# Performance work log

Hardware: AMD Instinct MI355X
Metric: run time of the kernel (lower is better)

Reference implementation:

```python
import jax, jax.numpy as jnp
import numpy as np

N, E, B, DIM = 10000, 100000, 64, 64
NF, EF, H = 92, 50, 128
N_CONV, STEPS = 2, 2


def setup_inputs() -> dict:
    key = jax.random.key(0)
    ks = jax.random.split(key, 16)
    r = lambda k, s: jax.random.normal(k, s, dtype=jnp.float32) * 0.05
    return {
        "x": jax.random.normal(ks[0], (N, NF), dtype=jnp.float32),
        "edge_attr": jax.random.normal(ks[1], (E, EF), dtype=jnp.float32),
        "lin0_w": r(ks[2], (DIM, NF)), "lin0_b": jnp.zeros((DIM,), jnp.float32),
        "nn1_w": r(ks[3], (H, EF)), "nn1_b": jnp.zeros((H,), jnp.float32),
        "nn2_w": r(ks[4], (DIM * DIM, H)), "nn2_b": jnp.zeros((DIM * DIM,), jnp.float32),
        "root": r(ks[5], (DIM, DIM)), "conv_bias": jnp.zeros((DIM,), jnp.float32),
        "gru_w_ih": r(ks[6], (3 * DIM, DIM)), "gru_w_hh": r(ks[7], (3 * DIM, DIM)),
        "gru_b_ih": jnp.zeros((3 * DIM,), jnp.float32), "gru_b_hh": jnp.zeros((3 * DIM,), jnp.float32),
        "lstm_w_ih": r(ks[8], (4 * DIM, 2 * DIM)), "lstm_w_hh": r(ks[9], (4 * DIM, DIM)),
        "lstm_b_ih": jnp.zeros((4 * DIM,), jnp.float32), "lstm_b_hh": jnp.zeros((4 * DIM,), jnp.float32),
        "lin1_w": r(ks[10], (DIM, 2 * DIM)), "lin1_b": jnp.zeros((DIM,), jnp.float32),
        "lin2_w": r(ks[11], (1, DIM)), "lin2_b": jnp.zeros((1,), jnp.float32),
        "edge_index": jax.random.randint(ks[12], (2, E), 0, N),
        "batch": jnp.sort(jax.random.randint(ks[13], (N,), 0, B)),
    }


def _forward(x, edge_attr, lin0_w, lin0_b, nn1_w, nn1_b, nn2_w, nn2_b, root, conv_bias,
             gru_w_ih, gru_w_hh, gru_b_ih, gru_b_hh, lstm_w_ih, lstm_w_hh, lstm_b_ih, lstm_b_hh,
             lin1_w, lin1_b, lin2_w, lin2_b, edge_index, batch):
    src, dst = edge_index[0], edge_index[1]
    out = jax.nn.relu(x @ lin0_w.T + lin0_b)            # [N, DIM]
    h = out                                              # GRU hidden state (h0 = out)
    # Edge-conditioned weights depend only on edge_attr; identical each conv step.
    he = jax.nn.relu(edge_attr @ nn1_w.T + nn1_b)        # [E, H]
    We = (he @ nn2_w.T + nn2_b).reshape(E, DIM, DIM)     # [E, DIM, DIM]
    deg = jax.ops.segment_sum(jnp.ones((E,), jnp.float32), dst, num_segments=N)
    inv_deg = jnp.where(deg > 0, 1.0 / jnp.maximum(deg, 1.0), 0.0)[:, None]
    for _ in range(N_CONV):
        msg = jnp.einsum('ei,eio->eo', out[src], We)     # per-edge matvec, [E, DIM]
        agg = jax.ops.segment_sum(msg, dst, num_segments=N) * inv_deg  # scatter-mean
        m = jax.nn.relu(agg + out @ root + conv_bias)
        # GRU cell (torch gate order: r, z, n)
        gx = m @ gru_w_ih.T + gru_b_ih
        gh = h @ gru_w_hh.T + gru_b_hh
        xr, xz, xn = jnp.split(gx, 3, axis=-1)
        hr, hz, hn = jnp.split(gh, 3, axis=-1)
        rg = jax.nn.sigmoid(xr + hr)
        zg = jax.nn.sigmoid(xz + hz)
        ng = jnp.tanh(xn + rg * hn)
        h = (1.0 - zg) * ng + zg * h
        out = h
    # Set2Set pooling
    q_star = jnp.zeros((B, 2 * DIM), jnp.float32)
    hs = jnp.zeros((B, DIM), jnp.float32)
    cs = jnp.zeros((B, DIM), jnp.float32)
    for _ in range(STEPS):
        gates = q_star @ lstm_w_ih.T + lstm_b_ih + hs @ lstm_w_hh.T + lstm_b_hh
        ig, fg, gg, og = jnp.split(gates, 4, axis=-1)    # torch gate order i,f,g,o
        cs = jax.nn.sigmoid(fg) * cs + jax.nn.sigmoid(ig) * jnp.tanh(gg)
        hs = jax.nn.sigmoid(og) * jnp.tanh(cs)
        q = hs                                           # [B, DIM]
        e = jnp.sum(out * q[batch], axis=-1)             # [N]
        emax = jax.ops.segment_max(e, batch, num_segments=B)
        ee = jnp.exp(e - emax[batch])
        denom = jax.ops.segment_sum(ee, batch, num_segments=B)
        a = ee / jnp.maximum(denom, 1e-16)[batch]        # per-graph softmax
        rvec = jax.ops.segment_sum(a[:, None] * out, batch, num_segments=B)
        q_star = jnp.concatenate([q, rvec], axis=-1)     # [B, 2*DIM]
    y = jax.nn.relu(q_star @ lin1_w.T + lin1_b) @ lin2_w.T + lin2_b
    return y.reshape(-1)                                 # [B]


def reference(x, edge_attr, lin0_w, lin0_b, nn1_w, nn1_b, nn2_w, nn2_b, root, conv_bias,
              gru_w_ih, gru_w_hh, gru_b_ih, gru_b_hh, lstm_w_ih, lstm_w_hh, lstm_b_ih, lstm_b_hh,
              lin1_w, lin1_b, lin2_w, lin2_b, edge_index, batch):
    return _forward(x, edge_attr, lin0_w, lin0_b, nn1_w, nn1_b, nn2_w, nn2_b, root, conv_bias,
                    gru_w_ih, gru_w_hh, gru_b_ih, gru_b_hh, lstm_w_ih, lstm_w_hh, lstm_b_ih, lstm_b_hh,
                    lin1_w, lin1_b, lin2_w, lin2_b, edge_index, batch)
```

## Files before the change

### kernel.cpp

```cpp
#include <hip/hip_runtime.h>
#include <hip/hip_bf16.h>

#define N_   10000
#define E_   100000
#define B_   64
#define DIM_ 64
#define NF_  92
#define EF_  50
#define H_   128

typedef unsigned int u32;

__device__ __forceinline__ float sigm(float x) { return 1.f / (1.f + __expf(-x)); }
__device__ __forceinline__ float rdlane(float v, int l) {
  return __uint_as_float(__builtin_amdgcn_readlane(__float_as_uint(v), l));
}

__global__ __launch_bounds__(256) void k_lin0(const float* __restrict__ x,
                                              const float* __restrict__ w,
                                              const float* __restrict__ b,
                                              float* __restrict__ out) {
  __shared__ float xs[4][NF_];
  __shared__ float w_s[DIM_][93];
  int n0 = blockIdx.x << 2;
  int tid = threadIdx.x;
  for (int k = tid; k < 4 * NF_; k += 256) {
    int nl = k / NF_, f = k % NF_;
    xs[nl][f] = x[(size_t)(n0 + nl) * NF_ + f];
  }
  for (int g = tid; g < DIM_ * NF_; g += 256) {
    int d = g / NF_, f = g % NF_;
    w_s[d][f] = w[g];
  }
  __syncthreads();
  int nl = tid >> 6, d = tid & 63;
  float acc = b[d];
  for (int f = 0; f < NF_; ++f) acc += xs[nl][f] * w_s[d][f];
  out[(size_t)(n0 + nl) * DIM_ + d] = fmaxf(acc, 0.f);
}

__global__ __launch_bounds__(256) void k_he(const float* __restrict__ ea,
                                            const float* __restrict__ w,
                                            const float* __restrict__ b,
                                            float* __restrict__ he) {
  __shared__ float wt[EF_][132];
  __shared__ float es[32][52];
  int e0 = blockIdx.x * 32, t = threadIdx.x;
  for (int g = t; g < H_ * EF_; g += 256) {
    int h = g / EF_, f = g % EF_;
    wt[f][h] = w[g];
  }
  for (int g = t; g < 32 * EF_; g += 256) {
    int e = g / EF_, f = g % EF_;
    es[e][f] = ea[(size_t)(e0 + e) * EF_ + f];
  }
  __syncthreads();
  int h0 = (t & 31) << 2, eg = t >> 5;
  float acc[4][4];
#pragma unroll
  for (int j = 0; j < 4; ++j)
#pragma unroll
    for (int c = 0; c < 4; ++c) acc[j][c] = b[h0 + c];
  for (int f = 0; f < EF_; ++f) {
    float4 wv = *(const float4*)&wt[f][h0];
    const float* wp = (const float*)&wv;
#pragma unroll
    for (int j = 0; j < 4; ++j) {
      float ev = es[eg * 4 + j][f];
#pragma unroll
      for (int c = 0; c < 4; ++c) acc[j][c] = fmaf(ev, wp[c], acc[j][c]);
    }
  }
#pragma unroll
  for (int j = 0; j < 4; ++j) {
    float4 o;
    o.x = fmaxf(acc[j][0], 0.f); o.y = fmaxf(acc[j][1], 0.f);
    o.z = fmaxf(acc[j][2], 0.f); o.w = fmaxf(acc[j][3], 0.f);
    *(float4*)&he[(size_t)(e0 + eg * 4 + j) * H_ + h0] = o;
  }
}

__global__ __launch_bounds__(256) void k_hist(const int* __restrict__ ei,
                                              int* __restrict__ outcnt,
                                              float* __restrict__ degf) {
  int e = blockIdx.x * 256 + threadIdx.x;
  if (e < E_) {
    atomicAdd(&outcnt[ei[e]], 1);
    atomicAdd(&degf[ei[E_ + e]], 1.0f);
  }
}

__global__ __launch_bounds__(1024) void k_scan(const int* __restrict__ outcnt,
                                               int* __restrict__ estart,
                                               int* __restrict__ cursor) {
  __shared__ int part[1024];
  int t = threadIdx.x;
  int base = t * 10;
  int c[10];
  int s = 0;
#pragma unroll
  for (int j = 0; j < 10; ++j) {
    int idx = base + j;
    c[j] = (idx < N_) ? outcnt[idx] : 0;
    s += c[j];
  }
  part[t] = s;
  __syncthreads();
  for (int off = 1; off < 1024; off <<= 1) {
    int v = (t >= off) ? part[t - off] : 0;
    __syncthreads();
    part[t] += v;
    __syncthreads();
  }
  int ex = (t > 0) ? part[t - 1] : 0;
#pragma unroll
  for (int j = 0; j < 10; ++j) {
    int idx = base + j;
    if (idx < N_) { estart[idx] = ex; cursor[idx] = ex; }
    ex += c[j];
  }
  if (t == 1023) estart[N_] = part[1023];
}

__global__ __launch_bounds__(256) void k_scatter(const int* __restrict__ ei,
                                                 int* __restrict__ cursor,
                                                 int* __restrict__ eorder) {
  int e = blockIdx.x * 256 + threadIdx.x;
  if (e < E_) {
    int s = ei[e];
    int pos = atomicAdd(&cursor[s], 1);
    eorder[pos] = e;
  }
}

__global__ __launch_bounds__(256) void k_gstart(const int* __restrict__ batch,
                                                int* __restrict__ gs) {
  int n = blockIdx.x * 256 + threadIdx.x;
  if (n >= N_) return;
  int b = batch[n];
  if (n == 0) {
    for (int bb = 0; bb <= b; ++bb) gs[bb] = 0;
  } else {
    int pb = batch[n - 1];
    if (pb != b)
      for (int bb = pb + 1; bb <= b; ++bb) gs[bb] = n;
  }
  if (n == N_ - 1) {
    for (int bb = b + 1; bb <= B_; ++bb) gs[bb] = N_;
  }
}

__global__ __launch_bounds__(256) void k_transpose(const float* __restrict__ gih,
                                                   const float* __restrict__ ghh,
                                                   const float* __restrict__ lih,
                                                   const float* __restrict__ lhh,
                                                   float* __restrict__ gihT,
                                                   float* __restrict__ ghhT,
                                                   float* __restrict__ lihT,
                                                   float* __restrict__ lhhT) {
  int idx = blockIdx.x * 256 + threadIdx.x;
  if (idx < 192 * 64) {
    int r = idx >> 6, i = idx & 63;
    gihT[i * 192 + r] = gih[idx];
    ghhT[i * 192 + r] = ghh[idx];
  }
  if (idx < 256 * 128) {
    int r = idx >> 7, k = idx & 127;
    lihT[k * 256 + r] = lih[idx];
  }
  if (idx < 256 * 64) {
    int r = idx >> 6, k = idx & 63;
    lhhT[k * 256 + r] = lhh[idx];
  }
}

__global__ __launch_bounds__(256) void k_vgemm(const float* __restrict__ outv,
                                               const float* __restrict__ nn2w,
                                               float* __restrict__ V4,
                                               int h_base, int H4Cbuf, int lwHg) {
  __shared__ float a_s[128][64];
  __shared__ float b_s[64][128];
  int n0 = blockIdx.x << 7;
  int og = blockIdx.y >> lwHg;
  int hg = blockIdx.y & ((1 << lwHg) - 1);
  int o0 = og << 4;
  int h0 = h_base + (hg << 3);
  int t = threadIdx.x;
#pragma unroll
  for (int k = 0; k < 8; ++k) {
    int idx = t + (k << 8);
    int nl = idx >> 4, i0 = (idx & 15) << 2;
    float4 v = make_float4(0.f, 0.f, 0.f, 0.f);
    int n = n0 + nl;
    if (n < N_) v = *(const float4*)&outv[(size_t)n * 64 + i0];
    int sh = 2 * nl;
    int c0 = (i0 + sh) & 63;
    a_s[nl][c0] = v.x; a_s[nl][c0 + 1] = v.y;
    int c2 = (i0 + 2 + sh) & 63;
    a_s[nl][c2] = v.z; a_s[nl][c2 + 1] = v.w;
  }
#pragma unroll
  for (int k = 0; k < 8; ++k) {
    int idx = t + (k << 8);
    int i = idx >> 5, c0 = (idx & 31) << 2;
    int o = o0 + (c0 >> 3);
    int hh = h0 + (c0 & 7);
    *(float4*)&b_s[i][c0] = *(const float4*)&nn2w[((size_t)((i << 6) + o)) * 128 + hh];
  }
  __syncthreads();
  int tx = t & 15, ty = t >> 4;
  float acc[8][8];
#pragma unroll
  for (int r = 0; r < 8; ++r)
#pragma unroll
    for (int c = 0; c < 8; ++c) acc[r][c] = 0.f;
#pragma unroll 4
  for (int i = 0; i < 64; i += 2) {
    float2 a2[8];
#pragma unroll
    for (int r = 0; r < 8; ++r) {
      int row = ty * 8 + r;
      a2[r] = *(const float2*)&a_s[row][(i + 2 * row) & 63];
    }
    float4 b00 = *(const float4*)&b_s[i][tx << 2];
    float4 b01 = *(const float4*)&b_s[i][64 + (tx << 2)];
    float4 b10 = *(const float4*)&b_s[i + 1][tx << 2];
    float4 b11 = *(const float4*)&b_s[i + 1][64 + (tx << 2)];
    const float* p00 = (const float*)&b00;
    const float* p01 = (const float*)&b01;
    const float* p10 = (const float*)&b10;
    const float* p11 = (const float*)&b11;
#pragma unroll
    for (int r = 0; r < 8; ++r) {
      float ax = a2[r].x, ay = a2[r].y;
#pragma unroll
      for (int c = 0; c < 4; ++c) {
        acc[r][c]     = fmaf(ax, p00[c], acc[r][c]);
        acc[r][c]     = fmaf(ay, p10[c], acc[r][c]);
        acc[r][4 + c] = fmaf(ax, p01[c], acc[r][4 + c]);
        acc[r][4 + c] = fmaf(ay, p11[c], acc[r][4 + c]);
      }
    }
  }
  float4* V4v = (float4*)V4;
  int h4 = (hg << 1) + (tx & 1);
  int olo = o0 + (tx >> 1);
#pragma unroll
  for (int r = 0; r < 8; ++r) {
    int n = n0 + ty * 8 + r;
    if (n >= N_) continue;
    float4 lo = make_float4(acc[r][0], acc[r][1], acc[r][2], acc[r][3]);
    float4 hi = make_float4(acc[r][4], acc[r][5], acc[r][6], acc[r][7]);
    size_t base = ((size_t)n * H4Cbuf + h4) * 64;
    V4v[base + olo]     = lo;
    V4v[base + olo + 8] = hi;
  }
}

__global__ __launch_bounds__(256) void k_bt(const float* __restrict__ out,
                                            const float* __restrict__ nn2b,
                                            float* __restrict__ bt) {
  __shared__ float os[4][64];
  int n0 = blockIdx.x << 2;
  int tid = threadIdx.x;
  int nl = tid >> 6, o = tid & 63;
  os[nl][o] = out[(size_t)(n0 + nl) * 64 + o];
  __syncthreads();
  float acc = 0.f;
  for (int i = 0; i < 64; ++i) acc += os[nl][i] * nn2b[(i << 6) + o];
  bt[(size_t)(n0 + nl) * 64 + o] = acc;
}

template <int H4C>
__global__ __launch_bounds__(256) void k_edge(const float* __restrict__ V4,
                                              const float* __restrict__ he,
                                              const float* __restrict__ bt,
                                              const int* __restrict__ ei,
                                              const int* __restrict__ estart,
                                              const int* __restrict__ eorder,
                                              float* __restrict__ agg,
                                              int hofs) {
  int wid = threadIdx.x >> 6, lane = threadIdx.x & 63;
  int n = blockIdx.x * 4 + wid;
  if (n >= N_) return;
  int se = estart[n], ee = estart[n + 1];
  if (se == ee) return;
  const float4* vp = (const float4*)V4 + (size_t)n * H4C * 64 + lane;
  float4 v4[H4C];
#pragma unroll
  for (int h4 = 0; h4 < H4C; ++h4) v4[h4] = vp[(size_t)h4 * 64];
  float btv = (hofs == 0) ? bt[(size_t)n * 64 + lane] : 0.f;
  constexpr int CWm1 = 4 * H4C - 1;
  for (int q = se; q < ee; ++q) {
    int eid = eorder[q];
    int dst = ei[E_ + eid];
    const float* hep = &he[(size_t)eid * H_];
    float hh, hh2 = 0.f;
    if (H4C == 32) { hh = hep[lane]; hh2 = hep[64 + lane]; }
    else           { hh = hep[hofs + (lane & CWm1)]; }
    float acc = btv;
#pragma unroll
    for (int h4 = 0; h4 < H4C; ++h4) {
      const float* vv = (const float*)&v4[h4];
#pragma unroll
      for (int c = 0; c < 4; ++c) {
        int hl = h4 * 4 + c;
        float bh = (hl < 64) ? rdlane(hh, hl) : rdlane(hh2, hl - 64);
        acc = fmaf(bh, vv[c], acc);
      }
    }
    atomicAdd(&agg[(size_t)dst * 64 + lane], acc);
  }
}

__global__ __launch_bounds__(256) void k_update(const float* __restrict__ agg,
                                                const float* __restrict__ deg,
                                                const float* __restrict__ cur,
                                                const float* __restrict__ root,
                                                const float* __restrict__ cbias,
                                                const float* __restrict__ wihT,
                                                const float* __restrict__ whhT,
                                                const float* __restrict__ bih,
                                                const float* __restrict__ bhh,
                                                float* __restrict__ nxt) {
  __shared__ float outs[32][64];
  __shared__ float ms[32][64];
  int n0 = blockIdx.x << 5;
  int tid = threadIdx.x;
  int o = tid & 63, g = tid >> 6;
#pragma unroll
  for (int k = 0; k < 8; ++k) {
    int idx = tid + (k << 8);
    int nl = idx >> 6, i = idx & 63;
    int n = n0 + nl;
    outs[nl][i] = (n < N_) ? cur[(size_t)n * 64 + i] : 0.f;
  }
  __syncthreads();
  float acc[8];
  float cb = cbias[o];
#pragma unroll
  for (int j = 0; j < 8; ++j) {
    int n = n0 + (g << 3) + j;
    if (n < N_) {
      float dg = deg[n];
      float iv = dg > 0.f ? 1.f / dg : 0.f;
      acc[j] = agg[(size_t)n * 64 + o] * iv + cb;
    } else acc[j] = 0.f;
  }
  for (int i = 0; i < 64; ++i) {
    float r = root[(i << 6) + o];
#pragma unroll
    for (int j = 0; j < 8; ++j) acc[j] = fmaf(outs[(g << 3) + j][i], r, acc[j]);
  }
#pragma unroll
  for (int j = 0; j < 8; ++j) ms[(g << 3) + j][o] = fmaxf(acc[j], 0.f);
  __syncthreads();
  float xr[8], xz[8], xn[8], hr[8], hz[8], hn[8];
  {
    float br = bih[o], bz = bih[64 + o], bn = bih[128 + o];
    float dr = bhh[o], dz = bhh[64 + o], dn = bhh[128 + o];
#pragma unroll
    for (int j = 0; j < 8; ++j) {
      xr[j] = br; xz[j] = bz; xn[j] = bn;
      hr[j] = dr; hz[j] = dz; hn[j] = dn;
    }
  }
  for (int i = 0; i < 64; ++i) {
    const float* wi = &wihT[i * 192];
    const float* vi = &whhT[i * 192];
    float w0 = wi[o], w1 = wi[64 + o], w2 = wi[128 + o];
    float v0 = vi[o], v1 = vi[64 + o], v2 = vi[128 + o];
#pragma unroll
    for (int j = 0; j < 8; ++j) {
      int nl = (g << 3) + j;
      float mi = ms[nl][i], hi = outs[nl][i];
      xr[j] = fmaf(mi, w0, xr[j]);
      xz[j] = fmaf(mi, w1, xz[j]);
      xn[j] = fmaf(mi, w2, xn[j]);
      hr[j] = fmaf(hi, v0, hr[j]);
      hz[j] = fmaf(hi, v1, hz[j]);
      hn[j] = fmaf(hi, v2, hn[j]);
    }
  }
#pragma unroll
  for (int j = 0; j < 8; ++j) {
    int nl = (g << 3) + j;
    int n = n0 + nl;
    if (n < N_) {
      float rg = sigm(xr[j] + hr[j]);
      float zg = sigm(xz[j] + hz[j]);
      float ng = tanhf(xn[j] + rg * hn[j]);
      nxt[(size_t)n * 64 + o] = (1.f - zg) * ng + zg * outs[nl][o];
    }
  }
}

__global__ __launch_bounds__(256) void k_s2s(const float* __restrict__ out,
                                             const int* __restrict__ gs,
                                             float* __restrict__ qstar,
                                             float* __restrict__ hs,
                                             float* __restrict__ cs,
                                             const float* __restrict__ lihT,
                                             const float* __restrict__ lhhT,
                                             const float* __restrict__ bih,
                                             const float* __restrict__ bhh,
                                             const float* __restrict__ w1,
                                             const float* __restrict__ b1,
                                             const float* __restrict__ w2,
                                             const float* __restrict__ b2,
                                             float* __restrict__ y, int dofinal) {
  int b = blockIdx.x, tid = threadIdx.x;
  __shared__ float qs[128];
  __shared__ float hss[64];
  __shared__ float gsh[256];
  __shared__ float qv[64];
  __shared__ float rv[64];
  __shared__ float wred[4];
  __shared__ float rred[4][64];
  if (tid < 128) qs[tid] = qstar[b * 128 + tid];
  else if (tid < 192) hss[tid - 128] = hs[b * 64 + (tid - 128)];
  __syncthreads();
  {
    int r = tid;
    float acc = bih[r] + bhh[r];
    for (int k = 0; k < 128; ++k) acc += qs[k] * lihT[k * 256 + r];
    for (int k = 0; k < 64; ++k) acc += hss[k] * lhhT[k * 256 + r];
    gsh[r] = acc;
  }
  __syncthreads();
  if (tid < 64) {
    float ig = sigm(gsh[tid]), fg = sigm(gsh[64 + tid]);
    float gg = tanhf(gsh[128 + tid]), og = sigm(gsh[192 + tid]);
    float c = fg * cs[b * 64 + tid] + ig * gg;
    cs[b * 64 + tid] = c;
    float hv = og * tanhf(c);
    hs[b * 64 + tid] = hv;
    qv[tid] = hv;
  }
  __syncthreads();
  int wid = tid >> 6, l = tid & 63;
  int s = gs[b], e_ = gs[b + 1];
  float wmax = -3.4e38f;
  for (int n = s + wid; n < e_; n += 4) {
    float p = out[(size_t)n * 64 + l] * qv[l];
#pragma unroll
    for (int off = 32; off; off >>= 1) p += __shfl_xor(p, off);
    wmax = fmaxf(wmax, p);
  }
  if (l == 0) wred[wid] = wmax;
  __syncthreads();
  float gmax = fmaxf(fmaxf(wred[0], wred[1]), fmaxf(wred[2], wred[3]));
  __syncthreads();
  float dacc = 0.f, racc = 0.f;
  for (int n = s + wid; n < e_; n += 4) {
    float p = out[(size_t)n * 64 + l] * qv[l];
#pragma unroll
    for (int off = 32; off; off >>= 1) p += __shfl_xor(p, off);
    float ee = __expf(p - gmax);
    dacc += ee;
    racc += ee * out[(size_t)n * 64 + l];
  }
  rred[wid][l] = racc;
  if (l == 0) wred[wid] = dacc;
  __syncthreads();
  if (wid == 0) {
    float denom = wred[0] + wred[1] + wred[2] + wred[3];
    float r = (rred[0][l] + rred[1][l] + rred[2][l] + rred[3][l]) /
              fmaxf(denom, 1e-16f);
    rv[l] = r;
    qstar[b * 128 + l] = qv[l];
    qstar[b * 128 + 64 + l] = r;
  }
  if (dofinal) {
    __syncthreads();
    if (tid < 64) {
      float acc = b1[tid];
      for (int k = 0; k < 64; ++k) acc += qv[k] * w1[tid * 128 + k];
      for (int k = 0; k < 64; ++k) acc += rv[k] * w1[tid * 128 + 64 + k];
      float t1 = fmaxf(acc, 0.f) * w2[tid];
#pragma unroll
      for (int off = 32; off; off >>= 1) t1 += __shfl_xor(t1, off);
      if (tid == 0) y[b] = t1 + b2[0];
    }
  }
}

extern "C" void kernel_launch(void* const* d_in, const int* in_sizes, int n_in,
                              void* d_out, int out_size, void* d_ws, size_t ws_size,
                              hipStream_t stream) {
  const float* x        = (const float*)d_in[0];
  const float* ea       = (const float*)d_in[1];
  const float* lin0_w   = (const float*)d_in[2];
  const float* lin0_b   = (const float*)d_in[3];
  const float* nn1_w    = (const float*)d_in[4];
  const float* nn1_b    = (const float*)d_in[5];
  const float* nn2_w    = (const float*)d_in[6];
  const float* nn2_b    = (const float*)d_in[7];
  const float* root     = (const float*)d_in[8];
  const float* cbias    = (const float*)d_in[9];
  const float* gru_wih  = (const float*)d_in[10];
  const float* gru_whh  = (const float*)d_in[11];
  const float* gru_bih  = (const float*)d_in[12];
  const float* gru_bhh  = (const float*)d_in[13];
  const float* lstm_wih = (const float*)d_in[14];
  const float* lstm_whh = (const float*)d_in[15];
  const float* lstm_bih = (const float*)d_in[16];
  const float* lstm_bhh = (const float*)d_in[17];
  const float* lin1_w   = (const float*)d_in[18];
  const float* lin1_b   = (const float*)d_in[19];
  const float* lin2_w   = (const float*)d_in[20];
  const float* lin2_b   = (const float*)d_in[21];
  const int*   ei       = (const int*)d_in[22];
  const int*   batch    = (const int*)d_in[23];
  float* yout = (float*)d_out;
  (void)n_in; (void)in_sizes; (void)out_size;

  size_t off = 0;
  auto carve = [&](size_t bytes) -> void* {
    void* p = (char*)d_ws + off;
    off = (off + bytes + 255) & ~(size_t)255;
    return p;
  };
  float* deg    = (float*)carve((size_t)N_ * 4);
  int*   outcnt = (int*)carve((size_t)N_ * 4);
  float* qstar  = (float*)carve((size_t)B_ * 128 * 4);
  float* hs     = (float*)carve((size_t)B_ * 64 * 4);
  float* cs     = (float*)carve((size_t)B_ * 64 * 4);
  size_t zero_span = off;
  float* out_a  = (float*)carve((size_t)N_ * DIM_ * 4);
  float* out_b  = (float*)carve((size_t)N_ * DIM_ * 4);
  float* bt     = (float*)carve((size_t)N_ * DIM_ * 4);
  float* agg    = (float*)carve((size_t)N_ * DIM_ * 4);
  int*   estart = (int*)carve((size_t)(N_ + 1) * 4);
  int*   cursor = (int*)carve((size_t)N_ * 4);
  int*   eorder = (int*)carve((size_t)E_ * 4);
  int*   gs     = (int*)carve((size_t)(B_ + 1) * 4);
  float* gihT   = (float*)carve((size_t)192 * 64 * 4);
  float* ghhT   = (float*)carve((size_t)192 * 64 * 4);
  float* lihT   = (float*)carve((size_t)256 * 128 * 4);
  float* lhhT   = (float*)carve((size_t)256 * 64 * 4);
  float* he     = (float*)carve((size_t)E_ * H_ * 4);
  size_t common = off;
  int CW = 8;
  {
    const int cws[4] = {64, 32, 16, 8};
    for (int i = 0; i < 4; ++i) {
      size_t vb = (size_t)N_ * cws[i] * 64 * 4;
      if (common + vb <= ws_size) { CW = cws[i]; break; }
    }
  }
  float* V4 = (float*)carve((size_t)N_ * CW * 64 * 4);
  int nchunks = 128 / CW;
  int lwHg = __builtin_ctz(CW >> 3);
  int H4Cb = CW / 4;

  hipMemsetAsync(d_ws, 0, zero_span, stream);

  k_lin0<<<N_ / 4, 256, 0, stream>>>(x, lin0_w, lin0_b, out_a);
  k_he<<<E_ / 32, 256, 0, stream>>>(ea, nn1_w, nn1_b, he);
  k_hist<<<(E_ + 255) / 256, 256, 0, stream>>>(ei, outcnt, deg);
  k_scan<<<1, 1024, 0, stream>>>(outcnt, estart, cursor);
  k_scatter<<<(E_ + 255) / 256, 256, 0, stream>>>(ei, cursor, eorder);
  k_gstart<<<(N_ + 255) / 256, 256, 0, stream>>>(batch, gs);
  k_transpose<<<128, 256, 0, stream>>>(gru_wih, gru_whh, lstm_wih, lstm_whh,
                                       gihT, ghhT, lihT, lhhT);

  float* cur = out_a;
  float* nxt = out_b;
  int ntile = (N_ + 127) / 128;
  dim3 vg(ntile, 4 << lwHg);
  int egrid = (N_ + 3) / 4;
  for (int t = 0; t < 2; ++t) {
    hipMemsetAsync(agg, 0, (size_t)N_ * DIM_ * 4, stream);
    k_bt<<<N_ / 4, 256, 0, stream>>>(cur, nn2_b, bt);
    for (int chunk = 0; chunk < nchunks; ++chunk) {
      int h_base = chunk * CW;
      k_vgemm<<<vg, 256, 0, stream>>>(cur, nn2_w, V4, h_base, H4Cb, lwHg);
      switch (CW) {
        case 64:  k_edge<16><<<egrid, 256, 0, stream>>>(V4, he, bt, ei, estart, eorder, agg, h_base); break;
        case 32:  k_edge<8><<<egrid, 256, 0, stream>>>(V4, he, bt, ei, estart, eorder, agg, h_base); break;
        case 16:  k_edge<4><<<egrid, 256, 0, stream>>>(V4, he, bt, ei, estart, eorder, agg, h_base); break;
        default:  k_edge<2><<<egrid, 256, 0, stream>>>(V4, he, bt, ei, estart, eorder, agg, h_base); break;
      }
    }
    k_update<<<(N_ + 31) / 32, 256, 0, stream>>>(agg, deg, cur, root, cbias,
                                                 gihT, ghhT, gru_bih, gru_bhh, nxt);
    float* tmp = cur; cur = nxt; nxt = tmp;
  }

  k_s2s<<<B_, 256, 0, stream>>>(cur, gs, qstar, hs, cs, lihT, lhhT,
                                lstm_bih, lstm_bhh, lin1_w, lin1_b, lin2_w,
                                lin2_b, yout, 0);
  k_s2s<<<B_, 256, 0, stream>>>(cur, gs, qstar, hs, cs, lihT, lhhT,
                                lstm_bih, lstm_bhh, lin1_w, lin1_b, lin2_w,
                                lin2_b, yout, 1);
}
```

Before: 908.6 us.

## Replace FP32 node-weight GEMM with split-bf16 MFMA GEMM

Replaces the scalar FP32 shared-memory GEMM that builds per-node V tensors with a matrix-core kernel using bf16 MFMA instructions. Both operands are split into high and low bf16 parts (three MFMAs per tile) to approximate FP32 accuracy, and nn2_w is pre-transposed and pre-split once into a chunked layout. The activations are split each conv step by a new kernel. This trades extra conversion passes, extra workspace and a small loss of precision for much higher matrix throughput.

Measured after the change: 817.8 us. 1.11x faster.

```diff
diff --git a/kernel.cpp b/kernel.cpp
--- a/kernel.cpp
+++ b/kernel.cpp
@@ -8,12 +8,24 @@
 #define NF_  92
 #define EF_  50
 #define H_   128
+#define NPAD 10048
 
 typedef unsigned int u32;
+typedef unsigned short u16;
+typedef __attribute__((ext_vector_type(8))) short s16x8;
+typedef __attribute__((ext_vector_type(4))) float f32x4;
 
 __device__ __forceinline__ float sigm(float x) { return 1.f / (1.f + __expf(-x)); }
 __device__ __forceinline__ float rdlane(float v, int l) {
   return __uint_as_float(__builtin_amdgcn_readlane(__float_as_uint(v), l));
+}
+__device__ __forceinline__ float bf2f(u16 u) {
+  return __uint_as_float(((u32)u) << 16);
+}
+__device__ __forceinline__ u16 f2bf(float f) {
+  u32 u = __float_as_uint(f);
+  u32 r = (u + 0x7FFFu + ((u >> 16) & 1u)) >> 16;
+  return (u16)r;
 }
 
 __global__ __launch_bounds__(256) void k_lin0(const float* __restrict__ x,
@@ -174,87 +186,96 @@
   }
 }
 
-__global__ __launch_bounds__(256) void k_vgemm(const float* __restrict__ outv,
-                                               const float* __restrict__ nn2w,
-                                               float* __restrict__ V4,
-                                               int h_base, int H4Cbuf, int lwHg) {
-  __shared__ float a_s[128][64];
-  __shared__ float b_s[64][128];
-  int n0 = blockIdx.x << 7;
-  int og = blockIdx.y >> lwHg;
-  int hg = blockIdx.y & ((1 << lwHg) - 1);
-  int o0 = og << 4;
-  int h0 = h_base + (hg << 3);
-  int t = threadIdx.x;
-#pragma unroll
-  for (int k = 0; k < 8; ++k) {
-    int idx = t + (k << 8);
-    int nl = idx >> 4, i0 = (idx & 15) << 2;
-    float4 v = make_float4(0.f, 0.f, 0.f, 0.f);
-    int n = n0 + nl;
-    if (n < N_) v = *(const float4*)&outv[(size_t)n * 64 + i0];
-    int sh = 2 * nl;
-    int c0 = (i0 + sh) & 63;
-    a_s[nl][c0] = v.x; a_s[nl][c0 + 1] = v.y;
-    int c2 = (i0 + 2 + sh) & 63;
-    a_s[nl][c2] = v.z; a_s[nl][c2 + 1] = v.w;
-  }
-#pragma unroll
-  for (int k = 0; k < 8; ++k) {
-    int idx = t + (k << 8);
-    int i = idx >> 5, c0 = (idx & 31) << 2;
-    int o = o0 + (c0 >> 3);
-    int hh = h0 + (c0 & 7);
-    *(float4*)&b_s[i][c0] = *(const float4*)&nn2w[((size_t)((i << 6) + o)) * 128 + hh];
-  }
-  __syncthreads();
-  int tx = t & 15, ty = t >> 4;
-  float acc[8][8];
-#pragma unroll
-  for (int r = 0; r < 8; ++r)
-#pragma unroll
-    for (int c = 0; c < 8; ++c) acc[r][c] = 0.f;
-#pragma unroll 4
-  for (int i = 0; i < 64; i += 2) {
-    float2 a2[8];
-#pragma unroll
-    for (int r = 0; r < 8; ++r) {
-      int row = ty * 8 + r;
-      a2[r] = *(const float2*)&a_s[row][(i + 2 * row) & 63];
-    }
-    float4 b00 = *(const float4*)&b_s[i][tx << 2];
-    float4 b01 = *(const float4*)&b_s[i][64 + (tx << 2)];
-    float4 b10 = *(const float4*)&b_s[i + 1][tx << 2];
-    float4 b11 = *(const float4*)&b_s[i + 1][64 + (tx << 2)];
-    const float* p00 = (const float*)&b00;
-    const float* p01 = (const float*)&b01;
-    const float* p10 = (const float*)&b10;
-    const float* p11 = (const float*)&b11;
-#pragma unroll
-    for (int r = 0; r < 8; ++r) {
-      float ax = a2[r].x, ay = a2[r].y;
-#pragma unroll
-      for (int c = 0; c < 4; ++c) {
-        acc[r][c]     = fmaf(ax, p00[c], acc[r][c]);
-        acc[r][c]     = fmaf(ay, p10[c], acc[r][c]);
-        acc[r][4 + c] = fmaf(ax, p01[c], acc[r][4 + c]);
-        acc[r][4 + c] = fmaf(ay, p11[c], acc[r][4 + c]);
+__global__ __launch_bounds__(256) void k_prep_w(const float* __restrict__ w,
+                                                u16* __restrict__ bth,
+                                                u16* __restrict__ btl,
+                                                int CW) {
+  int idx = blockIdx.x * 256 + threadIdx.x;
+  if (idx >= 64 * 64 * 128) return;
+  int h = idx & 127;
+  int io = idx >> 7;
+  int o = io & 63;
+  int i = io >> 6;
+  int chunk = h / CW, hl = h % CW;
+  float v = w[idx];
+  u16 hh = f2bf(v);
+  float r = v - bf2f(hh);
+  size_t dst = (size_t)chunk * CW * 4096 + ((size_t)(hl * 64 + o)) * 64 + i;
+  bth[dst] = hh;
+  btl[dst] = f2bf(r);
+}
+
+__global__ __launch_bounds__(256) void k_split_a(const float* __restrict__ src,
+                                                 u16* __restrict__ hi,
+                                                 u16* __restrict__ lo) {
+  int idx = blockIdx.x * 256 + threadIdx.x;
+  if (idx >= NPAD * 64) return;
+  float v = (idx < N_ * 64) ? src[idx] : 0.f;
+  u16 h = f2bf(v);
+  float r = v - bf2f(h);
+  hi[idx] = h;
+  lo[idx] = f2bf(r);
+}
+
+__global__ __launch_bounds__(256) void k_vgemm_mfma(const u16* __restrict__ Ah,
+                                                    const u16* __restrict__ Al,
+                                                    const u16* __restrict__ BTh,
+                                                    const u16* __restrict__ BTl,
+                                                    float* __restrict__ V4,
+                                                    int H4Cb) {
+  int n0 = blockIdx.x << 6;
+  int by = blockIdx.y;
+  int tid = threadIdx.x;
+  int w = tid >> 6, l = tid & 63;
+  int lr = l & 15, lg = l >> 4;
+  int o0 = w << 4;
+  int h0 = by << 2;
+  f32x4 acc[4][4];
+#pragma unroll
+  for (int nt = 0; nt < 4; ++nt)
+#pragma unroll
+    for (int t = 0; t < 4; ++t) acc[nt][t] = (f32x4){0.f, 0.f, 0.f, 0.f};
+#pragma unroll
+  for (int ks = 0; ks < 2; ++ks) {
+    int kk = (lg << 3) + (ks << 5);
+    s16x8 ah[4], al[4];
+#pragma unroll
+    for (int nt = 0; nt < 4; ++nt) {
+      size_t ao = (size_t)(n0 + (nt << 4) + lr) * 64 + kk;
+      ah[nt] = *(const s16x8*)(Ah + ao);
+      al[nt] = *(const s16x8*)(Al + ao);
+    }
+    s16x8 bh[4], bl[4];
+#pragma unroll
+    for (int t = 0; t < 4; ++t) {
+      size_t bo = (size_t)(((h0 + t) << 6) + o0 + lr) * 64 + kk;
+      bh[t] = *(const s16x8*)(BTh + bo);
+      bl[t] = *(const s16x8*)(BTl + bo);
+    }
+#pragma unroll
+    for (int nt = 0; nt < 4; ++nt)
+#pragma unroll
+      for (int t = 0; t < 4; ++t) {
+        acc[nt][t] = __builtin_amdgcn_mfma_f32_16x16x32_bf16(ah[nt], bh[t], acc[nt][t], 0, 0, 0);
+        acc[nt][t] = __builtin_amdgcn_mfma_f32_16x16x32_bf16(ah[nt], bl[t], acc[nt][t], 0, 0, 0);
+        acc[nt][t] = __builtin_amdgcn_mfma_f32_16x16x32_bf16(al[nt], bh[t], acc[nt][t], 0, 0, 0);
       }
-    }
-  }
-  float4* V4v = (float4*)V4;
-  int h4 = (hg << 1) + (tx & 1);
-  int olo = o0 + (tx >> 1);
-#pragma unroll
-  for (int r = 0; r < 8; ++r) {
-    int n = n0 + ty * 8 + r;
-    if (n >= N_) continue;
-    float4 lo = make_float4(acc[r][0], acc[r][1], acc[r][2], acc[r][3]);
-    float4 hi = make_float4(acc[r][4], acc[r][5], acc[r][6], acc[r][7]);
-    size_t base = ((size_t)n * H4Cbuf + h4) * 64;
-    V4v[base + olo]     = lo;
-    V4v[base + olo + 8] = hi;
-  }
+  }
+  float4* out4 = (float4*)V4;
+#pragma unroll
+  for (int nt = 0; nt < 4; ++nt)
+#pragma unroll
+    for (int r = 0; r < 4; ++r) {
+      int n = n0 + (nt << 4) + (lg << 2) + r;
+      if (n < N_) {
+        float4 f;
+        f.x = acc[nt][0][r];
+        f.y = acc[nt][1][r];
+        f.z = acc[nt][2][r];
+        f.w = acc[nt][3][r];
+        out4[((size_t)n * H4Cb + by) * 64 + o0 + lr] = f;
+      }
+    }
 }
 
 __global__ __launch_bounds__(256) void k_bt(const float* __restrict__ out,
@@ -539,6 +560,10 @@
   float* ghhT   = (float*)carve((size_t)192 * 64 * 4);
   float* lihT   = (float*)carve((size_t)256 * 128 * 4);
   float* lhhT   = (float*)carve((size_t)256 * 64 * 4);
+  u16*   Ah     = (u16*)carve((size_t)NPAD * 64 * 2);
+  u16*   Al     = (u16*)carve((size_t)NPAD * 64 * 2);
+  u16*   BTh    = (u16*)carve((size_t)128 * 4096 * 2);
+  u16*   BTl    = (u16*)carve((size_t)128 * 4096 * 2);
   float* he     = (float*)carve((size_t)E_ * H_ * 4);
   size_t common = off;
   int CW = 8;
@@ -551,7 +576,6 @@
   }
   float* V4 = (float*)carve((size_t)N_ * CW * 64 * 4);
   int nchunks = 128 / CW;
-  int lwHg = __builtin_ctz(CW >> 3);
   int H4Cb = CW / 4;
 
   hipMemsetAsync(d_ws, 0, zero_span, stream);
@@ -564,18 +588,21 @@
   k_gstart<<<(N_ + 255) / 256, 256, 0, stream>>>(batch, gs);
   k_transpose<<<128, 256, 0, stream>>>(gru_wih, gru_whh, lstm_wih, lstm_whh,
                                        gihT, ghhT, lihT, lhhT);
+  k_prep_w<<<2048, 256, 0, stream>>>(nn2_w, BTh, BTl, CW);
 
   float* cur = out_a;
   float* nxt = out_b;
-  int ntile = (N_ + 127) / 128;
-  dim3 vg(ntile, 4 << lwHg);
   int egrid = (N_ + 3) / 4;
+  int nblk = NPAD / 64;
   for (int t = 0; t < 2; ++t) {
     hipMemsetAsync(agg, 0, (size_t)N_ * DIM_ * 4, stream);
     k_bt<<<N_ / 4, 256, 0, stream>>>(cur, nn2_b, bt);
+    k_split_a<<<(NPAD * 64 + 255) / 256, 256, 0, stream>>>(cur, Ah, Al);
     for (int chunk = 0; chunk < nchunks; ++chunk) {
       int h_base = chunk * CW;
-      k_vgemm<<<vg, 256, 0, stream>>>(cur, nn2_w, V4, h_base, H4Cb, lwHg);
+      size_t boff = (size_t)chunk * CW * 4096;
+      dim3 vg(nblk, H4Cb);
+      k_vgemm_mfma<<<vg, 256, 0, stream>>>(Ah, Al, BTh + boff, BTl + boff, V4, H4Cb);
       switch (CW) {
         case 64:  k_edge<16><<<egrid, 256, 0, stream>>>(V4, he, bt, ei, estart, eorder, agg, h_base); break;
         case 32:  k_edge<8><<<egrid, 256, 0, stream>>>(V4, he, bt, ei, estart, eorder, agg, h_base); break;
```
